# Kernel optimization log

Hardware: AMD Instinct MI355X
Metric: run time of the kernel (lower is better)

Reference implementation:

```python
import jax, jax.numpy as jnp
import numpy as np

D_MODEL = 2048
NUM_HEADS = 32
NUM_KV_HEADS = 8
D_K = D_MODEL // NUM_HEADS
B, S = 2, 2048


def setup_inputs() -> dict:
    key = jax.random.key(0)
    ks = jax.random.split(key, 6)
    sc = 1.0 / np.sqrt(D_MODEL)
    x = jax.random.normal(ks[0], (B, S, D_MODEL), dtype=jnp.float32)
    mask = jnp.tril(jnp.ones((S, S), dtype=jnp.float32))[None, None]  # [1,1,S,S]
    return {
        'x': x,
        'mask': mask,
        'Wq': jax.random.normal(ks[1], (D_MODEL, D_MODEL), jnp.float32) * sc,
        'bq': jnp.zeros((D_MODEL,), jnp.float32),
        'Wk': jax.random.normal(ks[2], (D_MODEL, NUM_KV_HEADS * D_K), jnp.float32) * sc,
        'bk': jnp.zeros((NUM_KV_HEADS * D_K,), jnp.float32),
        'Wv': jax.random.normal(ks[3], (D_MODEL, NUM_KV_HEADS * D_K), jnp.float32) * sc,
        'bv': jnp.zeros((NUM_KV_HEADS * D_K,), jnp.float32),
        'Wo': jax.random.normal(ks[4], (D_MODEL, D_MODEL), jnp.float32) * sc,
        'bo': jnp.zeros((D_MODEL,), jnp.float32),
    }


def reference(x, mask, Wq, bq, Wk, bk, Wv, bv, Wo, bo):
    b, s, _ = x.shape
    g = NUM_HEADS // NUM_KV_HEADS  # queries per kv head
    Q = (x @ Wq + bq).reshape(b, s, NUM_HEADS, D_K).transpose(0, 2, 1, 3)      # [b,h,s,dk]
    K = (x @ Wk + bk).reshape(b, s, NUM_KV_HEADS, D_K).transpose(0, 2, 1, 3)   # [b,kv,s,dk]
    V = (x @ Wv + bv).reshape(b, s, NUM_KV_HEADS, D_K).transpose(0, 2, 1, 3)
    # group queries per kv head instead of repeat_interleave on K/V
    Qg = Q.reshape(b, NUM_KV_HEADS, g, s, D_K)
    scores = jnp.einsum('bkgqd,bkld->bkgql', Qg, K) / np.sqrt(D_K)             # [b,kv,g,s,s]
    scores = jnp.where(mask[:, :, None] == 0, -1e9, scores)
    attn = jax.nn.softmax(scores, axis=-1)
    out = jnp.einsum('bkgql,bkld->bkgqd', attn, V)                              # [b,kv,g,s,dk]
    out = out.reshape(b, NUM_HEADS, s, D_K).transpose(0, 2, 1, 3).reshape(b, s, D_MODEL)
    return out @ Wo + bo
```

## Files before the change

### kernel.cpp

```cpp
#include <hip/hip_runtime.h>
#include <stdint.h>

typedef __bf16 bf16x8 __attribute__((ext_vector_type(8)));
typedef float  f32x4  __attribute__((ext_vector_type(4)));

__device__ __forceinline__ f32x4 mfma16(bf16x8 a, bf16x8 b, f32x4 c) {
    return __builtin_amdgcn_mfma_f32_16x16x32_bf16(a, b, c, 0, 0, 0);
}

__device__ __forceinline__ uint16_t f2bf(float f) {
    union { __bf16 b; uint16_t u; } cv; cv.b = (__bf16)f; return cv.u;
}

typedef __attribute__((address_space(3))) void as3_void;
typedef __attribute__((address_space(1))) void as1_void;
__device__ __forceinline__ void async_ld16(const void* g, void* l) {
    __builtin_amdgcn_global_load_lds((const as1_void*)g, (as3_void*)l, 16, 0, 0);
}


__global__ void convert_f32_bf16(const float* __restrict__ in, uint16_t* __restrict__ out, int n) {
    int i = (blockIdx.x * 256 + threadIdx.x) * 4;
    if (i >= n) return;
    float4 v = *(const float4*)(in + i);
    ushort4 o;
    o.x = f2bf(v.x); o.y = f2bf(v.y); o.z = f2bf(v.z); o.w = f2bf(v.w);
    *(ushort4*)(out + i) = o;
}

__global__ void transpose_f32_bf16(const float* __restrict__ in, uint16_t* __restrict__ out,
                                   int ldin, int out_off, int ldout) {
    __shared__ float tile[32][33];
    const int c0 = blockIdx.x << 5, r0 = blockIdx.y << 5;
    const int tx = threadIdx.x, ty = threadIdx.y;
#pragma unroll
    for (int i = 0; i < 4; ++i)
        tile[ty + i * 8][tx] = in[(size_t)(r0 + ty + i * 8) * ldin + c0 + tx];
    __syncthreads();
#pragma unroll
    for (int i = 0; i < 4; ++i)
        out[(size_t)(out_off + c0 + ty + i * 8) * ldout + r0 + tx] = f2bf(tile[tx][ty + i * 8]);
}

__global__ void transpose_v(const uint16_t* __restrict__ qkv, uint16_t* __restrict__ vt) {
    __shared__ uint16_t tile[32][33];
    const int c0 = blockIdx.x << 5, r0 = blockIdx.y << 5, b = blockIdx.z;
    const int tx = threadIdx.x, ty = threadIdx.y;
#pragma unroll
    for (int i = 0; i < 4; ++i)
        tile[ty + i * 8][tx] = qkv[(size_t)(b * 2048 + r0 + ty + i * 8) * 3072 + 2560 + c0 + tx];
    __syncthreads();
#pragma unroll
    for (int i = 0; i < 4; ++i)
        vt[(size_t)(b * 512 + c0 + ty + i * 8) * 2048 + r0 + tx] = tile[tx][ty + i * 8];
}

__global__ void concat_bias(const float* __restrict__ bq, const float* __restrict__ bk,
                            const float* __restrict__ bv, float* __restrict__ out) {
    int i = blockIdx.x * 256 + threadIdx.x;
    if (i >= 3072) return;
    out[i] = (i < 2048) ? bq[i] : (i < 2560 ? bk[i - 2048] : bv[i - 2560]);
}

template <bool F32OUT>
__global__ __launch_bounds__(256, 2)
void gemm_bt(const uint16_t* __restrict__ A, const uint16_t* __restrict__ Bt,
             const float* __restrict__ bias, void* __restrict__ Cout, int N, int K) {
    __shared__ __align__(16) uint16_t As[4096];
    __shared__ __align__(16) uint16_t Bs[4096];
    const int tid = threadIdx.x;
    const int wv = tid >> 6, ln = tid & 63;
    const int quad = ln >> 4, l16 = ln & 15;
    const int row0 = blockIdx.y << 7, col0 = blockIdx.x << 7;
    const int wm = wv >> 1, wn = wv & 1;

    const int p0 = tid, p1 = tid + 256;
    const int ar0 = p0 >> 2, ac0 = (p0 & 3) ^ ((ar0 ^ (ar0 >> 2)) & 3);
    const int ar1 = p1 >> 2, ac1 = (p1 & 3) ^ ((ar1 ^ (ar1 >> 2)) & 3);
    const uint16_t* gA0 = A + (size_t)(row0 + ar0) * K + (ac0 << 3);
    const uint16_t* gA1 = A + (size_t)(row0 + ar1) * K + (ac1 << 3);
    const uint16_t* gB0 = Bt + (size_t)(col0 + ar0) * K + (ac0 << 3);
    const uint16_t* gB1 = Bt + (size_t)(col0 + ar1) * K + (ac1 << 3);
    uint16_t* lA0 = As + (wv << 9);
    uint16_t* lA1 = As + 2048 + (wv << 9);
    uint16_t* lB0 = Bs + (wv << 9);
    uint16_t* lB1 = Bs + 2048 + (wv << 9);

    int a_off[4], b_off[4];
#pragma unroll
    for (int t = 0; t < 4; ++t) {
        int r = (wm << 6) + (t << 4) + l16;
        a_off[t] = (((r << 2) + (quad ^ ((r ^ (r >> 2)) & 3))) << 3);
        r = (wn << 6) + (t << 4) + l16;
        b_off[t] = (((r << 2) + (quad ^ ((r ^ (r >> 2)) & 3))) << 3);
    }

    f32x4 acc[4][4] = {};

    for (int k0 = 0; k0 < K; k0 += 32) {
        __syncthreads();
        async_ld16(gA0 + k0, lA0);
        async_ld16(gA1 + k0, lA1);
        async_ld16(gB0 + k0, lB0);
        async_ld16(gB1 + k0, lB1);
        __syncthreads();
        bf16x8 af[4], bfr[4];
#pragma unroll
        for (int t = 0; t < 4; ++t) af[t] = *(const bf16x8*)(As + a_off[t]);
#pragma unroll
        for (int t = 0; t < 4; ++t) bfr[t] = *(const bf16x8*)(Bs + b_off[t]);
#pragma unroll
        for (int mt = 0; mt < 4; ++mt)
#pragma unroll
            for (int nt = 0; nt < 4; ++nt)
                acc[mt][nt] = mfma16(af[mt], bfr[nt], acc[mt][nt]);
    }

#pragma unroll
    for (int nt = 0; nt < 4; ++nt) {
        const int col = col0 + (wn << 6) + (nt << 4) + l16;
        const float bv = bias[col];
#pragma unroll
        for (int mt = 0; mt < 4; ++mt) {
            const int rbase = row0 + (wm << 6) + (mt << 4) + (quad << 2);
#pragma unroll
            for (int r = 0; r < 4; ++r) {
                float v = acc[mt][nt][r] + bv;
                if (F32OUT)
                    ((float*)Cout)[(size_t)(rbase + r) * N + col] = v;
                else
                    ((uint16_t*)Cout)[(size_t)(rbase + r) * N + col] = f2bf(v);
            }
        }
    }
}

__global__ __launch_bounds__(256, 2)
void attn_fwd(const uint16_t* __restrict__ QKV, const uint16_t* __restrict__ Vt,
              uint16_t* __restrict__ AO) {
    __shared__ __align__(16) uint16_t Ks[2][2048];
    __shared__ __align__(16) uint16_t Vs[2][2048];
    __shared__ __align__(16) uint16_t Ps[4][1280];

    const int tid = threadIdx.x;
    const int wv = tid >> 6, ln = tid & 63;
    const int quad = ln >> 4, l16 = ln & 15;
    const int p = blockIdx.x, kvh = blockIdx.y, b = blockIdx.z;
    const int h = kvh * 4 + wv;

    const uint16_t* Kg = QKV + (size_t)(b * 2048) * 3072 + 2048 + kvh * 64;
    const uint16_t* Vg = Vt + (size_t)(b * 512 + kvh * 64) * 2048;

    const int kr = tid >> 3, kc = (tid & 7) ^ (kr & 7);
    const int vr = tid >> 2, vc = (tid & 3) ^ ((vr ^ (vr >> 2)) & 3);
    const uint16_t* KgT = Kg + (size_t)kr * 3072 + kc * 8;
    const uint16_t* VgT = Vg + (size_t)vr * 2048 + vc * 8;

    int kf_off[2][2], vf_off[4];
#pragma unroll
    for (int nt = 0; nt < 2; ++nt)
#pragma unroll
        for (int kk = 0; kk < 2; ++kk) {
            int r = nt * 16 + l16, c = kk * 4 + quad;
            kf_off[nt][kk] = ((r << 3) + (c ^ (r & 7))) << 3;
        }
#pragma unroll
    for (int nt = 0; nt < 4; ++nt) {
        int r = nt * 16 + l16;
        vf_off[nt] = ((r << 2) + (quad ^ ((r ^ (r >> 2)) & 3))) << 3;
    }

#pragma unroll
    for (int half = 0; half < 2; ++half) {
        const int w = half ? (63 - p) : p;
        const int q0 = w << 5;

        bf16x8 qf[2][2];
#pragma unroll
        for (int mt = 0; mt < 2; ++mt)
#pragma unroll
            for (int kk = 0; kk < 2; ++kk)
                qf[mt][kk] = *(const bf16x8*)(QKV +
                    (size_t)(b * 2048 + q0 + mt * 16 + l16) * 3072 + h * 64 + kk * 32 + quad * 8);

        f32x4 acc[2][4] = {};
        float lpart[2][4] = {};

        const int nkb = w + 1;
        __syncthreads();
        async_ld16(KgT, Ks[0] + (wv << 9));
        async_ld16(VgT, Vs[0] + (wv << 9));

        for (int kb = 0; kb < nkb; ++kb) {
            const int cur = kb & 1;
            const int key0 = kb << 5;
            __syncthreads();
            if (kb + 1 < nkb) {
                async_ld16(KgT + ((kb + 1) << 5) * 3072, Ks[cur ^ 1] + (wv << 9));
                async_ld16(VgT + ((kb + 1) << 5), Vs[cur ^ 1] + (wv << 9));
            }

            bf16x8 kf[2][2];
#pragma unroll
            for (int nt = 0; nt < 2; ++nt)
#pragma unroll
                for (int kk = 0; kk < 2; ++kk)
                    kf[nt][kk] = *(const bf16x8*)(Ks[cur] + kf_off[nt][kk]);
            bf16x8 vf[4];
#pragma unroll
            for (int nt = 0; nt < 4; ++nt)
                vf[nt] = *(const bf16x8*)(Vs[cur] + vf_off[nt]);

            const bool diag = (kb == nkb - 1);
#pragma unroll
            for (int mt = 0; mt < 2; ++mt) {
                f32x4 s0 = {0.f, 0.f, 0.f, 0.f}, s1 = {0.f, 0.f, 0.f, 0.f};
                s0 = mfma16(qf[mt][0], kf[0][0], s0);
                s0 = mfma16(qf[mt][1], kf[0][1], s0);
                s1 = mfma16(qf[mt][0], kf[1][0], s1);
                s1 = mfma16(qf[mt][1], kf[1][1], s1);
#pragma unroll
                for (int r = 0; r < 4; ++r) {
                    float e0 = __expf(fmaf(s0[r], 0.125f, -16.0f));
                    float e1 = __expf(fmaf(s1[r], 0.125f, -16.0f));
                    if (diag) {
                        const int qrow = q0 + mt * 16 + quad * 4 + r;
                        if (key0 + l16 > qrow) e0 = 0.0f;
                        if (key0 + 16 + l16 > qrow) e1 = 0.0f;
                    }
                    lpart[mt][r] += e0 + e1;
                    const int prow = mt * 16 + quad * 4 + r;
                    Ps[wv][prow * 40 + l16] = f2bf(e0);
                    Ps[wv][prow * 40 + 16 + l16] = f2bf(e1);
                }
            }
#pragma unroll
            for (int mt = 0; mt < 2; ++mt) {
                bf16x8 pf = *(const bf16x8*)(&Ps[wv][(mt * 16 + l16) * 40 + quad * 8]);
#pragma unroll
                for (int nt = 0; nt < 4; ++nt)
                    acc[mt][nt] = mfma16(pf, vf[nt], acc[mt][nt]);
            }
        }

#pragma unroll
        for (int mt = 0; mt < 2; ++mt) {
            float inv[4];
#pragma unroll
            for (int r = 0; r < 4; ++r) {
                float rs = lpart[mt][r];
#pragma unroll
                for (int off = 1; off < 16; off <<= 1)
                    rs += __shfl_xor(rs, off, 64);
                inv[r] = 1.0f / rs;
            }
#pragma unroll
            for (int nt = 0; nt < 4; ++nt)
#pragma unroll
                for (int r = 0; r < 4; ++r) {
                    const int qrow = q0 + mt * 16 + quad * 4 + r;
                    AO[(size_t)(b * 2048 + qrow) * 2048 + h * 64 + nt * 16 + l16] =
                        f2bf(acc[mt][nt][r] * inv[r]);
                }
        }
    }
}


extern "C" void kernel_launch(void* const* d_in, const int* in_sizes, int n_in,
                              void* d_out, int out_size, void* d_ws, size_t ws_size,
                              hipStream_t stream) {
    (void)in_sizes; (void)n_in; (void)out_size; (void)ws_size;
    const float* x  = (const float*)d_in[0];
    const float* Wq = (const float*)d_in[2];
    const float* bq = (const float*)d_in[3];
    const float* Wk = (const float*)d_in[4];
    const float* bk = (const float*)d_in[5];
    const float* Wv = (const float*)d_in[6];
    const float* bv = (const float*)d_in[7];
    const float* Wo = (const float*)d_in[8];
    const float* bo = (const float*)d_in[9];

    char* ws = (char*)d_ws;
    uint16_t* xb    = (uint16_t*)ws;
    uint16_t* wqkvT = (uint16_t*)(ws + 16777216);
    uint16_t* woT   = (uint16_t*)(ws + 16777216 + 12582912);
    float*    biasq = (float*)(ws + 16777216 + 12582912 + 8388608);
    uint16_t* qkv   = (uint16_t*)d_out;
    uint16_t* ao    = xb;
    uint16_t* vt    = wqkvT;

    dim3 tb(32, 8);
    convert_f32_bf16<<<8192, 256, 0, stream>>>(x, xb, 4096 * 2048);
    transpose_f32_bf16<<<dim3(64, 64), tb, 0, stream>>>(Wq, wqkvT, 2048, 0,    2048);
    transpose_f32_bf16<<<dim3(16, 64), tb, 0, stream>>>(Wk, wqkvT, 512,  2048, 2048);
    transpose_f32_bf16<<<dim3(16, 64), tb, 0, stream>>>(Wv, wqkvT, 512,  2560, 2048);
    transpose_f32_bf16<<<dim3(64, 64), tb, 0, stream>>>(Wo, woT,   2048, 0,    2048);
    concat_bias<<<12, 256, 0, stream>>>(bq, bk, bv, biasq);

    gemm_bt<false><<<dim3(24, 32), 256, 0, stream>>>(xb, wqkvT, biasq, qkv, 3072, 2048);
    transpose_v<<<dim3(16, 64, 2), tb, 0, stream>>>(qkv, vt);
    attn_fwd<<<dim3(32, 8, 2), 256, 0, stream>>>(qkv, vt, ao);
    gemm_bt<true><<<dim3(16, 32), 256, 0, stream>>>(ao, woT, bo, d_out, 2048, 2048);
}
```

Before: 329.2 us.

## Halve attention query tile to 16 rows and double grid size

Each attention block now handles 16 query rows per head instead of 32, and the grid doubles from 32 to 64 blocks along the query axis, with paired query tiles kept for causal load balance. Launch bounds rise to 4 blocks per CU and the P staging buffer is halved to reduce register and LDS pressure. The goal is more blocks and higher occupancy for better latency hiding. The cost is that K/V tiles are loaded and synchronised twice as often per query row, which lowers data reuse, and the diagonal tile now wastes half its work on masked keys.

```diff
diff --git a/kernel.cpp b/kernel.cpp
--- a/kernel.cpp
+++ b/kernel.cpp
@@ -135,12 +135,12 @@
     }
 }
 
-__global__ __launch_bounds__(256, 2)
+__global__ __launch_bounds__(256, 4)
 void attn_fwd(const uint16_t* __restrict__ QKV, const uint16_t* __restrict__ Vt,
               uint16_t* __restrict__ AO) {
     __shared__ __align__(16) uint16_t Ks[2][2048];
     __shared__ __align__(16) uint16_t Vs[2][2048];
-    __shared__ __align__(16) uint16_t Ps[4][1280];
+    __shared__ __align__(16) uint16_t Ps[4][640];
 
     const int tid = threadIdx.x;
     const int wv = tid >> 6, ln = tid & 63;
@@ -172,21 +172,19 @@
 
 #pragma unroll
     for (int half = 0; half < 2; ++half) {
-        const int w = half ? (63 - p) : p;
-        const int q0 = w << 5;
-
-        bf16x8 qf[2][2];
-#pragma unroll
-        for (int mt = 0; mt < 2; ++mt)
-#pragma unroll
-            for (int kk = 0; kk < 2; ++kk)
-                qf[mt][kk] = *(const bf16x8*)(QKV +
-                    (size_t)(b * 2048 + q0 + mt * 16 + l16) * 3072 + h * 64 + kk * 32 + quad * 8);
-
-        f32x4 acc[2][4] = {};
-        float lpart[2][4] = {};
-
-        const int nkb = w + 1;
+        const int w = half ? (127 - p) : p;
+        const int q0 = w << 4;
+
+        bf16x8 qf[2];
+#pragma unroll
+        for (int kk = 0; kk < 2; ++kk)
+            qf[kk] = *(const bf16x8*)(QKV +
+                (size_t)(b * 2048 + q0 + l16) * 3072 + h * 64 + kk * 32 + quad * 8);
+
+        f32x4 acc[4] = {};
+        float lpart[4] = {};
+
+        const int nkb = (w >> 1) + 1;
         __syncthreads();
         async_ld16(KgT, Ks[0] + (wv << 9));
         async_ld16(VgT, Vs[0] + (wv << 9));
@@ -196,7 +194,7 @@
             const int key0 = kb << 5;
             __syncthreads();
             if (kb + 1 < nkb) {
-                async_ld16(KgT + ((kb + 1) << 5) * 3072, Ks[cur ^ 1] + (wv << 9));
+                async_ld16(KgT + (size_t)((kb + 1) << 5) * 3072, Ks[cur ^ 1] + (wv << 9));
                 async_ld16(VgT + ((kb + 1) << 5), Vs[cur ^ 1] + (wv << 9));
             }
 
@@ -211,58 +209,50 @@
             for (int nt = 0; nt < 4; ++nt)
                 vf[nt] = *(const bf16x8*)(Vs[cur] + vf_off[nt]);
 
+            f32x4 s0 = {0.f, 0.f, 0.f, 0.f}, s1 = {0.f, 0.f, 0.f, 0.f};
+            s0 = mfma16(qf[0], kf[0][0], s0);
+            s0 = mfma16(qf[1], kf[0][1], s0);
+            s1 = mfma16(qf[0], kf[1][0], s1);
+            s1 = mfma16(qf[1], kf[1][1], s1);
+
             const bool diag = (kb == nkb - 1);
 #pragma unroll
-            for (int mt = 0; mt < 2; ++mt) {
-                f32x4 s0 = {0.f, 0.f, 0.f, 0.f}, s1 = {0.f, 0.f, 0.f, 0.f};
-                s0 = mfma16(qf[mt][0], kf[0][0], s0);
-                s0 = mfma16(qf[mt][1], kf[0][1], s0);
-                s1 = mfma16(qf[mt][0], kf[1][0], s1);
-                s1 = mfma16(qf[mt][1], kf[1][1], s1);
-#pragma unroll
-                for (int r = 0; r < 4; ++r) {
-                    float e0 = __expf(fmaf(s0[r], 0.125f, -16.0f));
-                    float e1 = __expf(fmaf(s1[r], 0.125f, -16.0f));
-                    if (diag) {
-                        const int qrow = q0 + mt * 16 + quad * 4 + r;
-                        if (key0 + l16 > qrow) e0 = 0.0f;
-                        if (key0 + 16 + l16 > qrow) e1 = 0.0f;
-                    }
-                    lpart[mt][r] += e0 + e1;
-                    const int prow = mt * 16 + quad * 4 + r;
-                    Ps[wv][prow * 40 + l16] = f2bf(e0);
-                    Ps[wv][prow * 40 + 16 + l16] = f2bf(e1);
+            for (int r = 0; r < 4; ++r) {
+                float e0 = __expf(fmaf(s0[r], 0.125f, -16.0f));
+                float e1 = __expf(fmaf(s1[r], 0.125f, -16.0f));
+                if (diag) {
+                    const int qrow = q0 + quad * 4 + r;
+                    if (key0 + l16 > qrow) e0 = 0.0f;
+                    if (key0 + 16 + l16 > qrow) e1 = 0.0f;
                 }
-            }
-#pragma unroll
-            for (int mt = 0; mt < 2; ++mt) {
-                bf16x8 pf = *(const bf16x8*)(&Ps[wv][(mt * 16 + l16) * 40 + quad * 8]);
-#pragma unroll
-                for (int nt = 0; nt < 4; ++nt)
-                    acc[mt][nt] = mfma16(pf, vf[nt], acc[mt][nt]);
-            }
-        }
-
-#pragma unroll
-        for (int mt = 0; mt < 2; ++mt) {
-            float inv[4];
+                lpart[r] += e0 + e1;
+                const int prow = quad * 4 + r;
+                Ps[wv][prow * 40 + l16] = f2bf(e0);
+                Ps[wv][prow * 40 + 16 + l16] = f2bf(e1);
+            }
+            bf16x8 pf = *(const bf16x8*)(&Ps[wv][l16 * 40 + quad * 8]);
+#pragma unroll
+            for (int nt = 0; nt < 4; ++nt)
+                acc[nt] = mfma16(pf, vf[nt], acc[nt]);
+        }
+
+        float inv[4];
+#pragma unroll
+        for (int r = 0; r < 4; ++r) {
+            float rs = lpart[r];
+#pragma unroll
+            for (int off = 1; off < 16; off <<= 1)
+                rs += __shfl_xor(rs, off, 64);
+            inv[r] = 1.0f / rs;
+        }
+#pragma unroll
+        for (int nt = 0; nt < 4; ++nt)
 #pragma unroll
             for (int r = 0; r < 4; ++r) {
-                float rs = lpart[mt][r];
-#pragma unroll
-                for (int off = 1; off < 16; off <<= 1)
-                    rs += __shfl_xor(rs, off, 64);
-                inv[r] = 1.0f / rs;
-            }
-#pragma unroll
-            for (int nt = 0; nt < 4; ++nt)
-#pragma unroll
-                for (int r = 0; r < 4; ++r) {
-                    const int qrow = q0 + mt * 16 + quad * 4 + r;
-                    AO[(size_t)(b * 2048 + qrow) * 2048 + h * 64 + nt * 16 + l16] =
-                        f2bf(acc[mt][nt][r] * inv[r]);
-                }
-        }
+                const int qrow = q0 + quad * 4 + r;
+                AO[(size_t)(b * 2048 + qrow) * 2048 + h * 64 + nt * 16 + l16] =
+                    f2bf(acc[nt][r] * inv[r]);
+            }
     }
 }
 
@@ -300,6 +290,6 @@
 
     gemm_bt<false><<<dim3(24, 32), 256, 0, stream>>>(xb, wqkvT, biasq, qkv, 3072, 2048);
     transpose_v<<<dim3(16, 64, 2), tb, 0, stream>>>(qkv, vt);
-    attn_fwd<<<dim3(32, 8, 2), 256, 0, stream>>>(qkv, vt, ao);
+    attn_fwd<<<dim3(64, 8, 2), 256, 0, stream>>>(qkv, vt, ao);
     gemm_bt<true><<<dim3(16, 32), 256, 0, stream>>>(ao, woT, bo, d_out, 2048, 2048);
 }
```

New measurement: 329.6 us. About the same (+0.1%).
